# Kernel optimization log

Measured on AMD Instinct MI355X. Metric: run time of the kernel, lower is better.

The kernel has to match this reference:

```python
import jax, jax.numpy as jnp
import numpy as np

N, T, E, H, V = 32768, 20, 50, 50, 200
PAD = 0

def setup_inputs() -> dict:
    key = jax.random.key(0)
    ks = jax.random.split(key, 11)
    s = 1.0 / np.sqrt(H)  # torch LSTM init scale
    return {
        "char_indices": jax.random.randint(ks[0], (N, T), 0, V, dtype=jnp.int32),
        "word_lengths": jax.random.randint(ks[1], (N,), 0, T + 1, dtype=jnp.int32),
        "emb": jax.random.normal(ks[2], (V, E), jnp.float32) * 0.1,
        "W_ih_f": jax.random.normal(ks[3], (4 * H, E), jnp.float32) * s,
        "W_hh_f": jax.random.normal(ks[4], (4 * H, H), jnp.float32) * s,
        "b_ih_f": jax.random.normal(ks[5], (4 * H,), jnp.float32) * s,
        "b_hh_f": jax.random.normal(ks[6], (4 * H,), jnp.float32) * s,
        "W_ih_b": jax.random.normal(ks[7], (4 * H, E), jnp.float32) * s,
        "W_hh_b": jax.random.normal(ks[8], (4 * H, H), jnp.float32) * s,
        "b_ih_b": jax.random.normal(ks[9], (4 * H,), jnp.float32) * s,
        "b_hh_b": jax.random.normal(ks[10], (4 * H,), jnp.float32) * s,
    }

def _run_dir(x, lengths, W_ih, W_hh, b_ih, b_hh, reverse):
    # x: [N,T,E]; returns final hidden state [N,H] at the word's true boundary.
    n = x.shape[0]
    xg = jnp.einsum('nte,ge->ntg', x, W_ih) + b_ih + b_hh  # [N,T,4H]
    def step(carry, t):
        h, c = carry
        g = xg[:, t] + h @ W_hh.T  # [N,4H]
        i, f, gg, o = jnp.split(g, 4, axis=-1)
        c_new = jax.nn.sigmoid(f) * c + jax.nn.sigmoid(i) * jnp.tanh(gg)
        h_new = jax.nn.sigmoid(o) * jnp.tanh(c_new)
        valid = (t < lengths)[:, None]  # only update inside the word
        return (jnp.where(valid, h_new, h), jnp.where(valid, c_new, c)), None
    ts = jnp.arange(T - 1, -1, -1) if reverse else jnp.arange(T)
    z = jnp.zeros((n, W_hh.shape[1]), x.dtype)
    (h, _), _ = jax.lax.scan(step, (z, z), ts)
    return h

def reference(char_indices, word_lengths, emb, W_ih_f, W_hh_f, b_ih_f, b_hh_f,
              W_ih_b, W_hh_b, b_ih_b, b_hh_b):
    emb = emb.at[PAD].set(0.0)  # padding_idx row is zero
    x = emb[char_indices]  # [N,T,E]
    h_f = _run_dir(x, word_lengths, W_ih_f, W_hh_f, b_ih_f, b_hh_f, reverse=False)
    h_b = _run_dir(x, word_lengths, W_ih_b, W_hh_b, b_ih_b, b_hh_b, reverse=True)
    return jnp.concatenate([h_f, h_b], axis=-1)  # [N, 2H]
```

## Files before the change

### kernel.cpp

```cpp
#include <hip/hip_runtime.h>


#define TT    20
#define HH    50
#define VV    200
#define TILES 13
#define GSTR  212
#define GSH   (VV * GSTR)
#define WSH   (TILES * 16 * 64)
#define NW    32768
#define NB_G  332
#define NB_H  128
#define NBLK  342

#define L2E      1.4426950408889634f
#define TWO_L2E  2.8853900817779268f

typedef __attribute__((ext_vector_type(8))) short bf16x8;
typedef __attribute__((ext_vector_type(4))) short s16x4;
typedef __attribute__((ext_vector_type(4))) float f32x4;

__device__ __forceinline__ float frcp(float x) { return __builtin_amdgcn_rcpf(x); }
__device__ __forceinline__ float fexp2(float x) { return __builtin_amdgcn_exp2f(x); }

__device__ __forceinline__ short f2bf(float x) {
    unsigned b = __builtin_bit_cast(unsigned, x);
    unsigned r = (b + 0x7FFFu + ((b >> 16) & 1u)) >> 16;
    return (short)r;
}
__device__ __forceinline__ float bf2f(short s) {
    return __builtin_bit_cast(float, ((unsigned)(unsigned short)s) << 16);
}

__global__ void k_prep(const float* __restrict__ emb,
                       const float* __restrict__ Wih_f, const float* __restrict__ bih_f,
                       const float* __restrict__ bhh_f,
                       const float* __restrict__ Wih_b, const float* __restrict__ bih_b,
                       const float* __restrict__ bhh_b,
                       const int* __restrict__ lens,
                       short* __restrict__ Gimg, int* __restrict__ cnt) {
    int blk = blockIdx.x;
    int tid = threadIdx.x;
    if (blk < NB_G) {
        int idx = blk * 256 + tid;
        if (idx >= 2 * GSH) return;
        int d = idx / GSH;
        int rem = idx % GSH;
        int v = rem / GSTR;
        int u = (rem % GSTR) >> 2;
        int g = idx & 3;
        if (u >= HH) { Gimg[idx] = 0; return; }
        int r = g * HH + u;
        const float* Wih = d ? Wih_b : Wih_f;
        const float* bih = d ? bih_b : bih_f;
        const float* bhh = d ? bhh_b : bhh_f;
        float s = bih[r] + bhh[r];
        if (v != 0) {
            #pragma unroll 10
            for (int e = 0; e < HH; ++e) s = fmaf(emb[v * HH + e], Wih[r * HH + e], s);
        }
        s *= (g == 2) ? TWO_L2E : L2E;
        Gimg[idx] = f2bf(s);
    } else {
        int hb = blk - NB_G;
        __shared__ int hcnt[21];
        if (tid < 21) hcnt[tid] = 0;
        __syncthreads();
        atomicAdd(&hcnt[lens[hb * 256 + tid]], 1);
        __syncthreads();
        if (tid < 21) cnt[hb * 21 + tid] = hcnt[tid];
    }
}

__global__ void k_scat(const int* __restrict__ lens, const int* __restrict__ cnt,
                       int* __restrict__ perm) {
    __shared__ int tots[21], before_s[21], cur[21];
    int b = blockIdx.x, t = threadIdx.x;
    if (t < 21) {
        int before = 0, tot = 0;
        for (int bb = 0; bb < NB_H; ++bb) {
            int c = cnt[bb * 21 + t];
            before += (bb < b) ? c : 0;
            tot += c;
        }
        tots[t] = tot;
        before_s[t] = before;
    }
    __syncthreads();
    if (t < 21) {
        int start = 0;
        for (int L = 20; L > t; --L) start += tots[L];
        cur[t] = start + before_s[t];
    }
    __syncthreads();
    int i = b * 256 + t;
    int pos = atomicAdd(&cur[lens[i]], 1);
    perm[pos] = i;
}

__global__ void __launch_bounds__(768, 3)
k_lstm(const int* __restrict__ chars, const int* __restrict__ lens,
       const int* __restrict__ perm, const short* __restrict__ Gimg,
       const float* __restrict__ Whh_f, const float* __restrict__ Whh_b,
       float* __restrict__ out) {
    __shared__ __align__(16) short Wa[WSH];
    __shared__ __align__(16) short Gl[GSH];
    __shared__ __align__(16) short hs[12][1024];
    __shared__ unsigned char cs[12][320];

    int gb   = blockIdx.x;
    int d    = gb & 1;
    int grp  = gb >> 1;
    int tid  = threadIdx.x;
    int lane = tid & 63;
    int wv   = __builtin_amdgcn_readfirstlane(tid >> 6);
    int quad = lane >> 4;
    int n    = lane & 15;
    int x7   = n & 7;

    {
        const float* Whh = d ? Whh_b : Whh_f;
        for (int e = tid; e < WSH; e += 768) {
            int t = e >> 10, m = (e >> 6) & 15, k = e & 63;
            int u = 4 * t + (m >> 2), g = m & 3;
            float val = (k < HH && u < HH) ? Whh[(g * HH + u) * HH + k] : 0.0f;
            val *= (g == 2) ? TWO_L2E : L2E;
            int ksw = (k & 7) | (((k >> 3) ^ (m & 7)) << 3);
            Wa[(e & ~63) + ksw] = f2bf(val);
        }
    }
    {
        const int4* src = (const int4*)(Gimg + d * GSH);
        int4* dst = (int4*)Gl;
        for (int i = tid; i < GSH / 8; i += 768) dst[i] = src[i];
    }
    {
        int4 z = {0, 0, 0, 0};
        int4* hz = (int4*)&hs[0][0];
        for (int i = tid; i < 12 * 1024 / 8; i += 768) hz[i] = z;
    }
    int g = grp * 12 + wv;
    if (g > 2047) g = 2047;
    int slotbase = g * 16;
    {
        for (int i = lane; i < 16 * TT; i += 64) {
            int w = perm[slotbase + i / TT];
            cs[wv][i] = (unsigned char)chars[w * TT + i % TT];
        }
    }
    __syncthreads();

    int word = perm[slotbase + n];
    int L = lens[word];
    int mL = L;
    #pragma unroll
    for (int off = 8; off; off >>= 1) {
        int t2 = __shfl_xor(mL, off);
        mL = mL > t2 ? mL : t2;
    }
    mL = __builtin_amdgcn_readfirstlane(mL);

    const bf16x8* ap = (const bf16x8*)Wa;
    const bf16x8* bp = (const bf16x8*)hs[wv];
    short* hw = hs[wv];
    const unsigned char* cw = cs[wv] + n * TT;

    int pa0 = quad ^ x7;
    int pa1 = (quad + 4) ^ x7;

    float cst[TILES];
    #pragma unroll
    for (int t = 0; t < TILES; ++t) cst[t] = 0.0f;

    float* orow = out + (size_t)word * (2 * HH) + d * HH;

    #pragma unroll 1
    for (int s = 0; s < mL; ++s) {
        bool valid = s < L;
        int p = valid ? (d ? (L - 1 - s) : s) : 0;
        int v = cw[p];
        int grow = v * GSTR + quad * 4;

        bf16x8 B0 = bp[n * 8 + pa0];
        bf16x8 B1 = bp[n * 8 + pa1];

        f32x4 aN;
        {
            s16x4 gv = *(const s16x4*)&Gl[grow];
            f32x4 a;
            a[0] = bf2f(gv[0]); a[1] = bf2f(gv[1]);
            a[2] = bf2f(gv[2]); a[3] = bf2f(gv[3]);
            bf16x8 A0 = ap[n * 8 + pa0];
            bf16x8 A1 = ap[n * 8 + pa1];
            a = __builtin_amdgcn_mfma_f32_16x16x32_bf16(A0, B0, a, 0, 0, 0);
            aN = __builtin_amdgcn_mfma_f32_16x16x32_bf16(A1, B1, a, 0, 0, 0);
        }
        #pragma unroll
        for (int t = 0; t < TILES; ++t) {
            f32x4 ac = aN;
            if (t + 1 < TILES) {
                s16x4 gv = *(const s16x4*)&Gl[grow + (t + 1) * 16];
                f32x4 a;
                a[0] = bf2f(gv[0]); a[1] = bf2f(gv[1]);
                a[2] = bf2f(gv[2]); a[3] = bf2f(gv[3]);
                bf16x8 A0 = ap[((t + 1) * 16 + n) * 8 + pa0];
                bf16x8 A1 = ap[((t + 1) * 16 + n) * 8 + pa1];
                a = __builtin_amdgcn_mfma_f32_16x16x32_bf16(A0, B0, a, 0, 0, 0);
                aN = __builtin_amdgcn_mfma_f32_16x16x32_bf16(A1, B1, a, 0, 0, 0);
            }
            int u = 4 * t + quad;
            float ig = frcp(1.0f + fexp2(-ac[0]));
            float fg = frcp(1.0f + fexp2(-ac[1]));
            float og = frcp(1.0f + fexp2(-ac[3]));
            float gg = fmaf(-2.0f, frcp(1.0f + fexp2(ac[2])), 1.0f);
            float cn = fg * cst[t] + ig * gg;
            float th = fmaf(-2.0f, frcp(1.0f + fexp2(TWO_L2E * cn)), 1.0f);
            float hn = og * th;
            bool upd = valid && (u < HH);
            if (upd) {
                cst[t] = cn;
                int idx = n * 64 + (((u >> 3) ^ x7) << 3) + (u & 7);
                hw[idx] = f2bf(hn);
                if (s == L - 1) orow[u] = hn;
            }
        }
    }

    if (L == 0) {
        #pragma unroll
        for (int t = 0; t < TILES; ++t) {
            int u = 4 * t + quad;
            if (u < HH) orow[u] = 0.0f;
        }
    }
}

extern "C" void kernel_launch(void* const* d_in, const int* in_sizes, int n_in,
                              void* d_out, int out_size, void* d_ws, size_t ws_size,
                              hipStream_t stream) {
    const int*   chars = (const int*)d_in[0];
    const int*   lens  = (const int*)d_in[1];
    const float* emb   = (const float*)d_in[2];
    const float* Wih_f = (const float*)d_in[3];
    const float* Whh_f = (const float*)d_in[4];
    const float* bih_f = (const float*)d_in[5];
    const float* bhh_f = (const float*)d_in[6];
    const float* Wih_b = (const float*)d_in[7];
    const float* Whh_b = (const float*)d_in[8];
    const float* bih_b = (const float*)d_in[9];
    const float* bhh_b = (const float*)d_in[10];
    float* out = (float*)d_out;

    short* Gimg = (short*)d_ws;
    int*   cnt  = (int*)(Gimg + 2 * GSH);
    int*   perm = cnt + NB_H * 21;

    k_prep<<<NB_G + NB_H, 256, 0, stream>>>(emb, Wih_f, bih_f, bhh_f,
                                            Wih_b, bih_b, bhh_b, lens, Gimg, cnt);
    k_scat<<<NB_H, 256, 0, stream>>>(lens, cnt, perm);
    k_lstm<<<NBLK, 768, 0, stream>>>(chars, lens, perm, Gimg, Whh_f, Whh_b, out);
}
```

Measured before the change: 167.2 us.

## Hold recurrent weight fragments in registers, prebuild bf16 weight image in prep kernel

The scaled bf16 W_hh image is now built once by extra blocks in the prep kernel instead of by every LSTM block. Each wave then loads its MFMA A-operand fragments for all 13 tiles into registers before the time loop. This removes the shared-memory weight array and the per-step LDS reads of weights. The cost is about 104 extra VGPRs per lane, which may cause spills under the 768-thread launch bound, and a slightly larger prep launch.

Measured after the change: 166.8 us. Within noise of the previous version (-0.3%).

```diff
diff --git a/kernel.cpp b/kernel.cpp
--- a/kernel.cpp
+++ b/kernel.cpp
@@ -10,6 +10,7 @@
 #define WSH   (TILES * 16 * 64)
 #define NW    32768
 #define NB_G  332
+#define NB_W  104
 #define NB_H  128
 #define NBLK  342
 
@@ -37,8 +38,10 @@
                        const float* __restrict__ bhh_f,
                        const float* __restrict__ Wih_b, const float* __restrict__ bih_b,
                        const float* __restrict__ bhh_b,
+                       const float* __restrict__ Whh_f, const float* __restrict__ Whh_b,
                        const int* __restrict__ lens,
-                       short* __restrict__ Gimg, int* __restrict__ cnt) {
+                       short* __restrict__ Gimg, short* __restrict__ Wimg,
+                       int* __restrict__ cnt) {
     int blk = blockIdx.x;
     int tid = threadIdx.x;
     if (blk < NB_G) {
@@ -61,8 +64,18 @@
         }
         s *= (g == 2) ? TWO_L2E : L2E;
         Gimg[idx] = f2bf(s);
+    } else if (blk < NB_G + NB_W) {
+        int idx = (blk - NB_G) * 256 + tid;
+        int d = idx / WSH;
+        int e = idx % WSH;
+        int t = e >> 10, m = (e >> 6) & 15, k = e & 63;
+        int u = 4 * t + (m >> 2), g = m & 3;
+        const float* Whh = d ? Whh_b : Whh_f;
+        float val = (k < HH && u < HH) ? Whh[(g * HH + u) * HH + k] : 0.0f;
+        val *= (g == 2) ? TWO_L2E : L2E;
+        Wimg[idx] = f2bf(val);
     } else {
-        int hb = blk - NB_G;
+        int hb = blk - NB_G - NB_W;
         __shared__ int hcnt[21];
         if (tid < 21) hcnt[tid] = 0;
         __syncthreads();
@@ -101,9 +114,8 @@
 __global__ void __launch_bounds__(768, 3)
 k_lstm(const int* __restrict__ chars, const int* __restrict__ lens,
        const int* __restrict__ perm, const short* __restrict__ Gimg,
-       const float* __restrict__ Whh_f, const float* __restrict__ Whh_b,
+       const short* __restrict__ Wimg,
        float* __restrict__ out) {
-    __shared__ __align__(16) short Wa[WSH];
     __shared__ __align__(16) short Gl[GSH];
     __shared__ __align__(16) short hs[12][1024];
     __shared__ unsigned char cs[12][320];
@@ -119,17 +131,6 @@
     int x7   = n & 7;
 
     {
-        const float* Whh = d ? Whh_b : Whh_f;
-        for (int e = tid; e < WSH; e += 768) {
-            int t = e >> 10, m = (e >> 6) & 15, k = e & 63;
-            int u = 4 * t + (m >> 2), g = m & 3;
-            float val = (k < HH && u < HH) ? Whh[(g * HH + u) * HH + k] : 0.0f;
-            val *= (g == 2) ? TWO_L2E : L2E;
-            int ksw = (k & 7) | (((k >> 3) ^ (m & 7)) << 3);
-            Wa[(e & ~63) + ksw] = f2bf(val);
-        }
-    }
-    {
         const int4* src = (const int4*)(Gimg + d * GSH);
         int4* dst = (int4*)Gl;
         for (int i = tid; i < GSH / 8; i += 768) dst[i] = src[i];
@@ -148,6 +149,14 @@
             cs[wv][i] = (unsigned char)chars[w * TT + i % TT];
         }
     }
+
+    const bf16x8* wp = (const bf16x8*)(Wimg + d * WSH);
+    bf16x8 Af0[TILES], Af1[TILES];
+    #pragma unroll
+    for (int t = 0; t < TILES; ++t) {
+        Af0[t] = wp[(t * 16 + n) * 8 + quad];
+        Af1[t] = wp[(t * 16 + n) * 8 + 4 + quad];
+    }
     __syncthreads();
 
     int word = perm[slotbase + n];
@@ -160,7 +169,6 @@
     }
     mL = __builtin_amdgcn_readfirstlane(mL);
 
-    const bf16x8* ap = (const bf16x8*)Wa;
     const bf16x8* bp = (const bf16x8*)hs[wv];
     short* hw = hs[wv];
     const unsigned char* cw = cs[wv] + n * TT;
@@ -190,10 +198,8 @@
             f32x4 a;
             a[0] = bf2f(gv[0]); a[1] = bf2f(gv[1]);
             a[2] = bf2f(gv[2]); a[3] = bf2f(gv[3]);
-            bf16x8 A0 = ap[n * 8 + pa0];
-            bf16x8 A1 = ap[n * 8 + pa1];
-            a = __builtin_amdgcn_mfma_f32_16x16x32_bf16(A0, B0, a, 0, 0, 0);
-            aN = __builtin_amdgcn_mfma_f32_16x16x32_bf16(A1, B1, a, 0, 0, 0);
+            a = __builtin_amdgcn_mfma_f32_16x16x32_bf16(Af0[0], B0, a, 0, 0, 0);
+            aN = __builtin_amdgcn_mfma_f32_16x16x32_bf16(Af1[0], B1, a, 0, 0, 0);
         }
         #pragma unroll
         for (int t = 0; t < TILES; ++t) {
@@ -203,10 +209,8 @@
                 f32x4 a;
                 a[0] = bf2f(gv[0]); a[1] = bf2f(gv[1]);
                 a[2] = bf2f(gv[2]); a[3] = bf2f(gv[3]);
-                bf16x8 A0 = ap[((t + 1) * 16 + n) * 8 + pa0];
-                bf16x8 A1 = ap[((t + 1) * 16 + n) * 8 + pa1];
-                a = __builtin_amdgcn_mfma_f32_16x16x32_bf16(A0, B0, a, 0, 0, 0);
-                aN = __builtin_amdgcn_mfma_f32_16x16x32_bf16(A1, B1, a, 0, 0, 0);
+                a = __builtin_amdgcn_mfma_f32_16x16x32_bf16(Af0[t + 1], B0, a, 0, 0, 0);
+                aN = __builtin_amdgcn_mfma_f32_16x16x32_bf16(Af1[t + 1], B1, a, 0, 0, 0);
             }
             int u = 4 * t + quad;
             float ig = frcp(1.0f + fexp2(-ac[0]));
@@ -252,11 +256,14 @@
     float* out = (float*)d_out;
 
     short* Gimg = (short*)d_ws;
-    int*   cnt  = (int*)(Gimg + 2 * GSH);
+    short* Wimg = Gimg + 2 * GSH;
+    int*   cnt  = (int*)(Wimg + 2 * WSH);
     int*   perm = cnt + NB_H * 21;
 
-    k_prep<<<NB_G + NB_H, 256, 0, stream>>>(emb, Wih_f, bih_f, bhh_f,
-                                            Wih_b, bih_b, bhh_b, lens, Gimg, cnt);
+    k_prep<<<NB_G + NB_W + NB_H, 256, 0, stream>>>(emb, Wih_f, bih_f, bhh_f,
+                                                   Wih_b, bih_b, bhh_b,
+                                                   Whh_f, Whh_b, lens,
+                                                   Gimg, Wimg, cnt);
     k_scat<<<NB_H, 256, 0, stream>>>(lens, cnt, perm);
-    k_lstm<<<NBLK, 768, 0, stream>>>(chars, lens, perm, Gimg, Whh_f, Whh_b, out);
-}
+    k_lstm<<<NBLK, 768, 0, stream>>>(chars, lens, perm, Gimg, Wimg, out);
+}
```
